# Kernel tuning notes

Hardware: AMD Instinct MI355X
Metric: run time of the kernel (lower is better)

The kernel has to match this reference:

```python
import jax, jax.numpy as jnp
import numpy as np

VOCAB = 32000
DIM = 1024
DEPTH = 4
SEQ = 512
HEADS = 16
NMB = 4
MAXMEM = NMB * SEQ  # 2048
RAMP = 128
COEF = 1e-06
B = 4
DH = DIM // HEADS


def _ln(x, g, b):
    mu = jnp.mean(x, axis=-1, keepdims=True)
    v = jnp.mean((x - mu) ** 2, axis=-1, keepdims=True)
    return (x - mu) / jnp.sqrt(v + 1e-5) * g + b


def setup_inputs() -> dict:
    key = jax.random.key(0)
    ks = jax.random.split(key, 24)
    s = 0.02
    inp = {
        'tokens': jax.random.randint(ks[0], (B, SEQ), 0, VOCAB),
        'mems': jax.random.normal(ks[1], (DEPTH, B, MAXMEM, DIM), jnp.float32) * s,
        'times': jax.random.randint(ks[2], (DEPTH, MAXMEM), 0, 4096, dtype=jnp.int32),
        'token_emb': jax.random.normal(ks[3], (VOCAB, DIM), jnp.float32) * s,
        'expire_W': jax.random.normal(ks[4], (DEPTH, DIM), jnp.float32) * s,
        'expire_b': jnp.full((DEPTH,), -float(MAXMEM), jnp.float32),  # torch init constant
        'ln1_g': jnp.ones((DEPTH, DIM), jnp.float32),
        'ln1_b': jnp.zeros((DEPTH, DIM), jnp.float32),
        'Wq': jax.random.normal(ks[5], (DEPTH, DIM, DIM), jnp.float32) * s,
        'Wkv': jax.random.normal(ks[6], (DEPTH, DIM, 2 * DIM), jnp.float32) * s,
        'Wo': jax.random.normal(ks[7], (DEPTH, DIM, DIM), jnp.float32) * s,
        'bo': jnp.zeros((DEPTH, DIM), jnp.float32),
        'ln2_g': jnp.ones((DEPTH, DIM), jnp.float32),
        'ln2_b': jnp.zeros((DEPTH, DIM), jnp.float32),
        'W1': jax.random.normal(ks[8], (DEPTH, DIM, 4 * DIM), jnp.float32) * s,
        'b1': jnp.zeros((DEPTH, 4 * DIM), jnp.float32),
        'W2': jax.random.normal(ks[9], (DEPTH, 4 * DIM, DIM), jnp.float32) * s,
        'b2': jnp.zeros((DEPTH, DIM), jnp.float32),
        'logits_W': jax.random.normal(ks[10], (DIM, VOCAB), jnp.float32) * s,
        'logits_b': jnp.zeros((VOCAB,), jnp.float32),
    }
    return inp


def reference(tokens, mems, times, token_emb, expire_W, expire_b, ln1_g, ln1_b,
              Wq, Wkv, Wo, bo, ln2_g, ln2_b, W1, b1, W2, b2, logits_W, logits_b):
    n, M = SEQ, MAXMEM
    scale = DH ** -0.5
    x = token_emb[tokens]  # (B, n, DIM)
    # causal mask over concat(mem, x): query i may attend key j iff j <= i + M
    causal = jnp.triu(jnp.ones((n, M + n), bool), k=M + 1)  # True = masked
    aux = jnp.float32(0.0)
    new_mems, new_times = [], []
    tnew = jnp.arange(n - 1, -1, -1, dtype=times.dtype)
    for d in range(DEPTH):
        mem = mems[d]                       # (B, M, DIM)
        t = times[d].astype(jnp.float32)    # (M,)
        hidden = x
        # --- expire span: per-memory-slot soft retention mask ---
        exps = jax.nn.sigmoid(mem @ expire_W[d] + expire_b[d]) * M  # (B, M)
        r = exps[:, None, None, :] - t[None, None, None, :]          # (B,1,1,M)
        r = jnp.pad(r, ((0, 0), (0, 0), (0, 0), (0, n)), constant_values=1.0)
        emask = jnp.clip(r / RAMP + 1.0, 0.0, 1.0)                   # (B,1,1,M+n)
        # --- pre-norm causal attention over concat(mem, x_normed) ---
        xn = _ln(x, ln1_g[d], ln1_b[d])
        q = (xn @ Wq[d]).reshape(B, n, HEADS, DH).transpose(0, 2, 1, 3)
        ctx = jnp.concatenate([mem, xn], axis=1)                     # (B, M+n, DIM)
        kv = ctx @ Wkv[d]
        k = kv[..., :DIM].reshape(B, M + n, HEADS, DH).transpose(0, 2, 1, 3)
        v = kv[..., DIM:].reshape(B, M + n, HEADS, DH).transpose(0, 2, 1, 3)
        dots = jnp.einsum('bhid,bhjd->bhij', q, k) * scale
        dots = jnp.where(causal, -jnp.inf, dots)
        attn = jax.nn.softmax(dots, axis=-1) * emask
        out = jnp.einsum('bhij,bhjd->bhid', attn, v)
        out = out.transpose(0, 2, 1, 3).reshape(B, n, DIM)
        x = out @ Wo[d] + bo[d] + x
        # --- pre-norm FFN ---
        xn2 = _ln(x, ln2_g[d], ln2_b[d])
        x = jax.nn.gelu(xn2 @ W1[d] + b1[d], approximate=False) @ W2[d] + b2[d] + x
        aux = aux + (exps / SEQ).sum() * COEF
        # --- memory bookkeeping (detached) ---
        new_mems.append(jax.lax.stop_gradient(
            jnp.concatenate([mem, hidden], axis=1)[:, -M:]))
        new_times.append(jnp.concatenate([times[d] + n, tnew])[-M:])
    logits = x @ logits_W + logits_b
    return (logits, jnp.stack(new_mems), jnp.stack(new_times), aux)
```

## Files before the change

kernel.cpp:

```cpp
#include <hip/hip_runtime.h>
#include <cmath>

#define DIMC   1024
#define SEQC   512
#define BC     4
#define MC     2048
#define CTXC   2560
#define HEADSC 16
#define DHC    64
#define VOCABC 32000
#define MAXC   512

using short8 = __attribute__((ext_vector_type(8))) short;
using f32x4  = __attribute__((ext_vector_type(4))) float;
using u16x4  = __attribute__((ext_vector_type(4))) unsigned short;
using u16x8  = __attribute__((ext_vector_type(8))) unsigned short;

__device__ __forceinline__ unsigned short f2bf(float f) {
    unsigned u = __float_as_uint(f);
    unsigned r = (u + 0x7fffu + ((u >> 16) & 1u)) >> 16;
    return (unsigned short)r;
}

__device__ __forceinline__ void glds16(const unsigned short* g, char* l) {
    __builtin_amdgcn_global_load_lds(
        (const __attribute__((address_space(1))) void*)g,
        (__attribute__((address_space(3))) void*)l, 16, 0, 0);
}

__global__ __launch_bounds__(256) void embed_kernel(const int* __restrict__ tokens,
                                                    const float* __restrict__ emb,
                                                    float* __restrict__ x) {
    int row = blockIdx.x;
    int tok = tokens[row];
    const float4 v = *(const float4*)(emb + (size_t)tok * DIMC + threadIdx.x * 4);
    *(float4*)(x + (size_t)row * DIMC + threadIdx.x * 4) = v;
}

__global__ __launch_bounds__(256) void times_init_kernel(const int* __restrict__ times,
                                                         float* __restrict__ out_times,
                                                         float* __restrict__ aux) {
    int i = blockIdx.x * 256 + threadIdx.x;
    if (i == 0) aux[0] = 0.0f;
    if (i < 4 * MC) {
        int d = i >> 11, m = i & (MC - 1);
        out_times[i] = (m < MC - SEQC) ? (float)(times[d * MC + SEQC + m] + SEQC)
                                       : (float)(MC - 1 - m);
    }
}

#define PREP_MEM 8192
#define PREP_XC  10240
#define PREP_LN  12288
#define PREP_TOT 24576
__global__ __launch_bounds__(256) void prep_kernel(
    const float* __restrict__ mem_d, const float* __restrict__ x,
    const float* __restrict__ eW, const float* __restrict__ eb,
    float* __restrict__ exps, float* __restrict__ aux,
    unsigned short* __restrict__ mem_b, float* __restrict__ out_mems_d,
    const float* __restrict__ g1, const float* __restrict__ b1v,
    unsigned short* __restrict__ xn_b,
    const float* __restrict__ Wq, const float* __restrict__ Wkv,
    const float* __restrict__ Wo, const float* __restrict__ W1,
    const float* __restrict__ W2,
    unsigned short* __restrict__ wq_t, unsigned short* __restrict__ wkv_t,
    unsigned short* __restrict__ wo_t, unsigned short* __restrict__ w1_t,
    unsigned short* __restrict__ w2_t) {
    __shared__ float sh[1056];
    const int bid = blockIdx.x, tid = threadIdx.x;
    if (bid < PREP_MEM) {
        int row = bid;
        int m = row & 2047, b = row >> 11;
        const float4 v = *(const float4*)(mem_d + (size_t)row * DIMC + tid * 4);
        const float4 w = *(const float4*)(eW + tid * 4);
        float s = v.x * w.x + v.y * w.y + v.z * w.z + v.w * w.w;
        for (int off = 32; off; off >>= 1) s += __shfl_down(s, off, 64);
        int wid = tid >> 6, lane = tid & 63;
        if (lane == 0) sh[wid] = s;
        u16x4 o = { f2bf(v.x), f2bf(v.y), f2bf(v.z), f2bf(v.w) };
        *(u16x4*)(mem_b + (size_t)row * DIMC + tid * 4) = o;
        if (m >= SEQC)
            *(float4*)(out_mems_d + ((size_t)(b * MC + m - SEQC)) * DIMC + tid * 4) = v;
        __syncthreads();
        if (tid == 0) {
            float z = sh[0] + sh[1] + sh[2] + sh[3] + eb[0];
            float e = (float)MC / (1.0f + expf(-z));
            exps[row] = e;
            atomicAdd(aux, e * (1e-6f / (float)SEQC));
        }
    } else if (bid < PREP_XC) {
        int r = bid - PREP_MEM;
        int b = r >> 9, i = r & 511;
        const float4 v = *(const float4*)(x + (size_t)r * DIMC + tid * 4);
        *(float4*)(out_mems_d + ((size_t)(b * MC + MC - SEQC + i)) * DIMC + tid * 4) = v;
    } else if (bid < PREP_LN) {
        int row = bid - PREP_XC;
        const float4 v = *(const float4*)(x + (size_t)row * DIMC + tid * 4);
        float s = v.x + v.y + v.z + v.w;
        float q = v.x * v.x + v.y * v.y + v.z * v.z + v.w * v.w;
        for (int off = 32; off; off >>= 1) {
            s += __shfl_down(s, off, 64);
            q += __shfl_down(q, off, 64);
        }
        int wid = tid >> 6, lane = tid & 63;
        if (lane == 0) { sh[wid] = s; sh[4 + wid] = q; }
        __syncthreads();
        if (tid == 0) {
            float S = sh[0] + sh[1] + sh[2] + sh[3];
            float Q = sh[4] + sh[5] + sh[6] + sh[7];
            float mu = S / DIMC;
            float var = Q / DIMC - mu * mu;
            sh[8] = mu;
            sh[9] = rsqrtf(var + 1e-5f);
        }
        __syncthreads();
        float mu = sh[8], rstd = sh[9];
        const float4 gg = *(const float4*)(g1 + tid * 4);
        const float4 bb = *(const float4*)(b1v + tid * 4);
        u16x4 o = { f2bf((v.x - mu) * rstd * gg.x + bb.x),
                    f2bf((v.y - mu) * rstd * gg.y + bb.y),
                    f2bf((v.z - mu) * rstd * gg.z + bb.z),
                    f2bf((v.w - mu) * rstd * gg.w + bb.w) };
        *(u16x4*)(xn_b + (size_t)row * DIMC + tid * 4) = o;
    } else {
        int t = bid - PREP_LN;
        const float* W; unsigned short* Wt; int K, N, tx, ty;
        if (t < 1024)      { W = Wq;  Wt = wq_t;  K = 1024; N = 1024; tx = t & 31;  ty = t >> 5; }
        else if (t < 3072) { int u = t - 1024; W = Wkv; Wt = wkv_t; K = 1024; N = 2048; tx = u & 63;  ty = u >> 6; }
        else if (t < 4096) { int u = t - 3072; W = Wo;  Wt = wo_t;  K = 1024; N = 1024; tx = u & 31;  ty = u >> 5; }
        else if (t < 8192) { int u = t - 4096; W = W1;  Wt = w1_t;  K = 1024; N = 4096; tx = u & 127; ty = u >> 7; }
        else               { int u = t - 8192; W = W2;  Wt = w2_t;  K = 4096; N = 1024; tx = u & 31;  ty = u >> 5; }
        int n0 = tx * 32, k0 = ty * 32;
        int r = tid >> 3, c = (tid & 7) * 4;
        const float4 v = *(const float4*)(W + (size_t)(k0 + r) * N + n0 + c);
        sh[r * 33 + c] = v.x; sh[r * 33 + c + 1] = v.y;
        sh[r * 33 + c + 2] = v.z; sh[r * 33 + c + 3] = v.w;
        __syncthreads();
        u16x4 o = { f2bf(sh[(c + 0) * 33 + r]), f2bf(sh[(c + 1) * 33 + r]),
                    f2bf(sh[(c + 2) * 33 + r]), f2bf(sh[(c + 3) * 33 + r]) };
        *(u16x4*)(Wt + (size_t)(n0 + r) * K + k0 + c) = o;
    }
}

__global__ __launch_bounds__(64) void compact_kernel(
    const float* __restrict__ exps, const int* __restrict__ times_d,
    int* __restrict__ cidx, float* __restrict__ em_c, int* __restrict__ cnt) {
    int b = blockIdx.x, lane = threadIdx.x;
    int c = 0;
    for (int it = 0; it < 32; ++it) {
        int j = it * 64 + lane;
        float e = exps[b * MC + j];
        float rr = (e - (float)times_d[j]) * (1.0f / 128.0f) + 1.0f;
        float em = fminf(fmaxf(rr, 0.0f), 1.0f);
        unsigned long long mk = __ballot(em > 0.0f);
        int pos = c + __popcll(mk & ((1ull << lane) - 1ull));
        if (em > 0.0f) {
            cidx[b * 2048 + pos] = j;
            em_c[b * 2048 + pos] = em;
        }
        c += __popcll(mk);
    }
    int padded = (c + 63) & ~63;
    int fill_to = padded < MAXC ? MAXC : padded;
    for (int p = c + lane; p < fill_to; p += 64) {
        cidx[b * 2048 + p] = 0;
        em_c[b * 2048 + p] = 0.0f;
    }
    int tiles = padded >> 6;
    if (tiles > (MAXC >> 6)) tiles = MAXC >> 6;
    if (lane == 0) cnt[b] = tiles;
}

__global__ __launch_bounds__(256) void ln_kernel(const float* __restrict__ in,
                                                 const float* __restrict__ g,
                                                 const float* __restrict__ b,
                                                 unsigned short* __restrict__ outb) {
    int row = blockIdx.x;
    int tid = threadIdx.x;
    const float4 v = *(const float4*)(in + (size_t)row * DIMC + tid * 4);
    float s = v.x + v.y + v.z + v.w;
    float q = v.x * v.x + v.y * v.y + v.z * v.z + v.w * v.w;
    for (int off = 32; off; off >>= 1) {
        s += __shfl_down(s, off, 64);
        q += __shfl_down(q, off, 64);
    }
    __shared__ float ss[4], sq[4];
    int wid = tid >> 6, lane = tid & 63;
    if (lane == 0) { ss[wid] = s; sq[wid] = q; }
    __syncthreads();
    if (tid == 0) {
        float S = ss[0] + ss[1] + ss[2] + ss[3];
        float Q = sq[0] + sq[1] + sq[2] + sq[3];
        float mu = S / DIMC;
        float var = Q / DIMC - mu * mu;
        ss[0] = mu;
        sq[0] = rsqrtf(var + 1e-5f);
    }
    __syncthreads();
    float mu = ss[0], rstd = sq[0];
    const float4 gg = *(const float4*)(g + tid * 4);
    const float4 bb = *(const float4*)(b + tid * 4);
    u16x4 o = { f2bf((v.x - mu) * rstd * gg.x + bb.x),
                f2bf((v.y - mu) * rstd * gg.y + bb.y),
                f2bf((v.z - mu) * rstd * gg.z + bb.z),
                f2bf((v.w - mu) * rstd * gg.w + bb.w) };
    *(u16x4*)(outb + (size_t)row * DIMC + tid * 4) = o;
}

__global__ __launch_bounds__(256) void wt_kernel(const float* __restrict__ W,
                                                 unsigned short* __restrict__ Wt,
                                                 int K, int N) {
    __shared__ float t[32][33];
    int tid = threadIdx.x;
    int n0 = blockIdx.x * 32, k0 = blockIdx.y * 32;
    int r = tid >> 3, c = (tid & 7) * 4;
    const float4 v = *(const float4*)(W + (size_t)(k0 + r) * N + n0 + c);
    t[r][c] = v.x; t[r][c + 1] = v.y; t[r][c + 2] = v.z; t[r][c + 3] = v.w;
    __syncthreads();
    u16x4 o = { f2bf(t[c + 0][r]), f2bf(t[c + 1][r]),
                f2bf(t[c + 2][r]), f2bf(t[c + 3][r]) };
    *(u16x4*)(Wt + (size_t)(n0 + r) * K + k0 + c) = o;
}

__global__ __launch_bounds__(256) void vt_kernel(const unsigned short* __restrict__ kvb,
                                                 unsigned short* __restrict__ vT) {
    __shared__ unsigned short t[64][72];
    int jt = blockIdx.x, dt = blockIdx.y, b = blockIdx.z;
    int j0 = MC + jt * 64;
    int tid = threadIdx.x;
    int r = tid >> 3, c = (tid & 7) * 8;
    #pragma unroll
    for (int p = 0; p < 2; ++p) {
        u16x8 v = *(const u16x8*)(kvb + ((size_t)(b * CTXC + j0 + r + p * 32)) * 2048
                                  + 1024 + dt * 64 + c);
        *(u16x8*)&t[r + p * 32][c] = v;
    }
    __syncthreads();
    #pragma unroll
    for (int p = 0; p < 2; ++p) {
        int dr = r + p * 32;
        u16x8 o = { t[c + 0][dr], t[c + 1][dr], t[c + 2][dr], t[c + 3][dr],
                    t[c + 4][dr], t[c + 5][dr], t[c + 6][dr], t[c + 7][dr] };
        *(u16x8*)(vT + ((size_t)(b * 1024 + dt * 64 + dr)) * CTXC + j0 + c) = o;
    }
}

__global__ __launch_bounds__(256) void vtc_kernel(const unsigned short* __restrict__ kvc,
                                                  const int* __restrict__ cnt,
                                                  unsigned short* __restrict__ vTc) {
    int ct = blockIdx.x, dt = blockIdx.y, b = blockIdx.z;
    if (ct >= cnt[b]) return;
    __shared__ unsigned short t[64][72];
    int tid = threadIdx.x;
    int r = tid >> 3, c = (tid & 7) * 8;
    #pragma unroll
    for (int p = 0; p < 2; ++p) {
        u16x8 v = *(const u16x8*)(kvc + ((size_t)(b * MAXC + ct * 64 + r + p * 32)) * 1024
                                  + dt * 64 + c);
        *(u16x8*)&t[r + p * 32][c] = v;
    }
    __syncthreads();
    #pragma unroll
    for (int p = 0; p < 2; ++p) {
        int dr = r + p * 32;
        u16x8 o = { t[c + 0][dr], t[c + 1][dr], t[c + 2][dr], t[c + 3][dr],
                    t[c + 4][dr], t[c + 5][dr], t[c + 6][dr], t[c + 7][dr] };
        *(u16x8*)(vTc + ((size_t)(b * 1024 + dt * 64 + dr)) * MAXC + ct * 64 + c) = o;
    }
}

template<int AMODE, bool BIAS, bool GELU, bool RES, int OMODE, int RT>
__device__ __forceinline__ void gemm_body(
    unsigned short* As, unsigned short* Bs,
    const unsigned short* __restrict__ A, const int* __restrict__ gidx,
    const unsigned short* __restrict__ Wt, const float* __restrict__ bias,
    const float* __restrict__ res, float* __restrict__ Cf,
    unsigned short* __restrict__ Cb, int K, int N, int bx, int by) {
    constexpr int MF = RT / 32;
    const int tid = threadIdx.x;
    const int lane = tid & 63, wave = tid >> 6;
    const int row0 = by * RT, col0 = bx * 128;

    const int seg = tid & 3;
    const int rr0 = tid >> 2;
    const unsigned short* arow[RT / 64];
    #pragma unroll
    for (int p = 0; p < RT / 64; ++p) {
        int r = row0 + p * 64 + rr0;
        if (AMODE == 2) {
            int b = r >> 9, slot = r & (MAXC - 1);
            arow[p] = A + ((size_t)(b * 2048 + gidx[b * 2048 + slot])) * K;
        } else {
            arow[p] = A + (size_t)r * K;
        }
        arow[p] += seg * 8;
    }
    const unsigned short* brow[2];
    #pragma unroll
    for (int p = 0; p < 2; ++p)
        brow[p] = Wt + (size_t)(col0 + p * 64 + rr0) * K + seg * 8;

    char* lA0 = (char*)As + (tid & 192) * 16;
    char* lB0 = (char*)Bs + (tid & 192) * 16;
    char* lB1 = lB0 + 4096;

    f32x4 acc[MF][4] = {};

    const int wr = (wave >> 1) * (RT / 2), wc = (wave & 1) * 64;
    const int fr = lane & 15;
    const int k8 = (lane >> 4) * 8;
    const unsigned short* Ar = As + (size_t)(wr + fr) * 32 + k8;
    const unsigned short* Br = Bs + (size_t)(wc + fr) * 32 + k8;

    for (int k0 = 0; k0 < K; k0 += 32) {
        glds16(arow[0] + k0, lA0);
        if (RT == 128) glds16(arow[1] + k0, lA0 + 4096);
        glds16(brow[0] + k0, lB0);
        glds16(brow[1] + k0, lB1);
        __syncthreads();
        short8 a[MF], b[4];
        #pragma unroll
        for (int m = 0; m < MF; ++m) a[m] = *(const short8*)(Ar + m * 16 * 32);
        #pragma unroll
        for (int n = 0; n < 4; ++n) b[n] = *(const short8*)(Br + n * 16 * 32);
        #pragma unroll
        for (int m = 0; m < MF; ++m)
            #pragma unroll
            for (int n = 0; n < 4; ++n)
                acc[m][n] = __builtin_amdgcn_mfma_f32_16x16x32_bf16(a[m], b[n], acc[m][n], 0, 0, 0);
        __syncthreads();
    }

    const int orow = row0 + wr + (lane >> 4) * 4;
    const int ocol = col0 + wc + fr;
    #pragma unroll
    for (int n = 0; n < 4; ++n) {
        int c = ocol + n * 16;
        float bv = BIAS ? bias[c] : 0.0f;
        #pragma unroll
        for (int m = 0; m < MF; ++m) {
            #pragma unroll
            for (int i = 0; i < 4; ++i) {
                int r0 = orow + m * 16 + i;
                size_t orr = r0;
                if (OMODE == 1) orr = (size_t)r0 + (size_t)(r0 >> 11) * 512;
                if (OMODE == 2) orr = (size_t)r0 + (size_t)(r0 >> 9) * 2048 + 2048;
                size_t idx = orr * N + c;
                float v = acc[m][n][i] + bv;
                if (GELU) v = 0.5f * v * (1.0f + erff(v * 0.70710678118f));
                if (RES) v += res[idx];
                if (Cf) Cf[idx] = v;
                if (Cb) Cb[idx] = f2bf(v);
            }
        }
    }
}

__global__ __launch_bounds__(256) void qkv_gemm_kernel(
    const unsigned short* __restrict__ xn_b, const unsigned short* __restrict__ mem_b,
    const unsigned short* __restrict__ wq_t, const unsigned short* __restrict__ wkv_t,
    const int* __restrict__ cidx, const int* __restrict__ cnt,
    unsigned short* __restrict__ qb, unsigned short* __restrict__ kvb,
    unsigned short* __restrict__ kvc) {
    __shared__ unsigned short As[128 * 32];
    __shared__ unsigned short Bs[128 * 32];
    int id = blockIdx.x;
    if (id < 128) {
        gemm_body<0, false, false, false, 0, 128>(As, Bs, xn_b, nullptr, wq_t,
            nullptr, nullptr, nullptr, qb, 1024, 1024, id & 7, id >> 3);
    } else if (id < 384) {
        id -= 128;
        gemm_body<0, false, false, false, 2, 128>(As, Bs, xn_b, nullptr, wkv_t,
            nullptr, nullptr, nullptr, kvb, 1024, 2048, id & 15, id >> 4);
    } else if (id < 896) {
        id -= 384;
        gemm_body<0, false, false, false, 1, 128>(As, Bs, mem_b, nullptr, wkv_t,
            nullptr, nullptr, nullptr, kvb, 1024, 2048, id & 7, id >> 3);
    } else {
        id -= 896;
        int by = id >> 3;
        int b = (by * 64) >> 9, slot0 = (by * 64) & (MAXC - 1);
        if (slot0 >= cnt[b] * 64) return;
        gemm_body<2, false, false, false, 0, 64>(As, Bs, mem_b, cidx,
            wkv_t + (size_t)1024 * 1024, nullptr, nullptr, nullptr, kvc,
            1024, 1024, id & 7, by);
    }
}

__global__ __launch_bounds__(256) void gemm64_kernel(
    const unsigned short* __restrict__ A, const unsigned short* __restrict__ Wt,
    const float* __restrict__ bias, const float* __restrict__ res,
    float* __restrict__ Cf, unsigned short* __restrict__ Cb, int K) {
    __shared__ unsigned short As[64 * 32];
    __shared__ unsigned short Bs[128 * 32];
    gemm_body<0, true, false, true, 0, 64>(As, Bs, A, nullptr, Wt, bias, res,
        Cf, Cb, K, 1024, blockIdx.x, blockIdx.y);
}

__global__ __launch_bounds__(256) void ffn1_kernel(
    const unsigned short* __restrict__ A, const unsigned short* __restrict__ Wt,
    const float* __restrict__ bias, unsigned short* __restrict__ Cb) {
    __shared__ unsigned short As[128 * 32];
    __shared__ unsigned short Bs[128 * 32];
    gemm_body<0, true, true, false, 0, 128>(As, Bs, A, nullptr, Wt, bias, nullptr,
        nullptr, Cb, 1024, 4096, blockIdx.x, blockIdx.y);
}

__global__ __launch_bounds__(256) void logits_kernel(
    const unsigned short* __restrict__ A, const unsigned short* __restrict__ Wt,
    const float* __restrict__ bias, float* __restrict__ Cf) {
    __shared__ unsigned short As[128 * 32];
    __shared__ unsigned short Bs[128 * 32];
    gemm_body<0, true, false, false, 0, 128>(As, Bs, A, nullptr, Wt, bias, nullptr,
        Cf, nullptr, 1024, VOCABC, blockIdx.y, blockIdx.x);
}

__global__ __launch_bounds__(512) void attn_mfma_kernel(
    const unsigned short* __restrict__ qb,
    const unsigned short* __restrict__ kvb,
    const unsigned short* __restrict__ vT,
    const unsigned short* __restrict__ vTc,
    const int* __restrict__ cidx,
    const float* __restrict__ em_c,
    const int* __restrict__ cnt,
    unsigned short* __restrict__ outb) {
    __shared__ unsigned short K_s[2][64 * 64];
    __shared__ unsigned short V_s[2][64 * 64];
    __shared__ unsigned short p_s[8][16][72];
    __shared__ float em_s[64];
    const int tid = threadIdx.x;
    const int lane = tid & 63, wave = tid >> 6;
    const int qt = blockIdx.x, h = blockIdx.y, b = blockIdx.z;
    const int fr = lane & 15, g = lane >> 4;
    const int gq = qt * 128 + wave * 16;

    short8 aq[2];
    {
        const unsigned short* qp = qb + ((size_t)(b * SEQC + gq + fr)) * DIMC + h * DHC + g * 8;
        aq[0] = *(const short8*)qp;
        aq[1] = *(const short8*)(qp + 32);
    }

    const int sr = tid >> 3, ss = tid & 7;
    const int sw = (ss ^ (sr & 7)) * 8;
    const int wbase = (tid & 448) * 16;

    f32x4 acc_o[4] = {};
    float m_q = -1e30f, l_q = 0.0f;

    const int nlt = 2 * (qt + 1);
    const int nt = 32 + nlt;

    auto stage12 = [&](int t, int q) {
        const int jbase = t * 64;
        glds16(kvb + ((size_t)(b * CTXC + jbase + sr)) * 2048 + h * DHC + sw,
               (char*)K_s[q] + wbase);
        if (t >= 32)
            glds16(vT + ((size_t)(b * 1024 + h * DHC + sr)) * CTXC + jbase + sw,
                   (char*)V_s[q] + wbase);
    };

    stage12(0, 0);
    asm volatile("s_waitcnt vmcnt(0)" ::: "memory");
    __builtin_amdgcn_s_barrier();
    int cur = 0;
    for (int t = 0; t < nt; ++t) {
        if (t + 1 < nt) stage12(t + 1, cur ^ 1);
        if (t + 1 >= nt)      asm volatile("s_waitcnt vmcnt(0)" ::: "memory");
        else if (t >= 31)     asm volatile("s_waitcnt vmcnt(2)" ::: "memory");
        else                  asm volatile("s_waitcnt vmcnt(1)" ::: "memory");
        __builtin_amdgcn_s_barrier();
        __builtin_amdgcn_sched_barrier(0);

        const bool live = (t < 32) || ((t - 32) * 64 <= gq + 15);
        if (live) {
            f32x4 sT[4] = {};
            #pragma unroll
            for (int ks = 0; ks < 2; ++ks)
                #pragma unroll
                for (int mf = 0; mf < 4; ++mf) {
                    int row = mf * 16 + fr, sg = (ks * 4 + g) ^ (row & 7);
                    short8 kk = *(const short8*)((const char*)K_s[cur] + row * 128 + sg * 16);
                    sT[mf] = __builtin_amdgcn_mfma_f32_16x16x32_bf16(kk, aq[ks], sT[mf], 0, 0, 0);
                }

            if (t < 32) {
                float mx = sT[0][0];
                #pragma unroll
                for (int mf = 0; mf < 4; ++mf)
                    #pragma unroll
                    for (int i = 0; i < 4; ++i) mx = fmaxf(mx, sT[mf][i]);
                mx *= 0.125f;
                mx = fmaxf(mx, __shfl_xor(mx, 16, 64));
                mx = fmaxf(mx, __shfl_xor(mx, 32, 64));
                float mnew = fmaxf(m_q, mx);
                float fs = __expf(m_q - mnew);
                m_q = mnew;
                float ps = 0.0f;
                #pragma unroll
                for (int mf = 0; mf < 4; ++mf)
                    #pragma unroll
                    for (int i = 0; i < 4; ++i)
                        ps += __expf(sT[mf][i] * 0.125f - mnew);
                ps += __shfl_xor(ps, 16, 64);
                ps += __shfl_xor(ps, 32, 64);
                l_q = l_q * fs + ps;
            } else {
                const int lt = t - 32;
                const int kq = gq + fr - lt * 64;
                float sv[4][4];
                #pragma unroll
                for (int mf = 0; mf < 4; ++mf)
                    #pragma unroll
                    for (int i = 0; i < 4; ++i) {
                        int kl = mf * 16 + g * 4 + i;
                        sv[mf][i] = (kl <= kq) ? sT[mf][i] * 0.125f : -1e30f;
                    }
                float mx = sv[0][0];
                #pragma unroll
                for (int mf = 0; mf < 4; ++mf)
                    #pragma unroll
                    for (int i = 0; i < 4; ++i) mx = fmaxf(mx, sv[mf][i]);
                mx = fmaxf(mx, __shfl_xor(mx, 16, 64));
                mx = fmaxf(mx, __shfl_xor(mx, 32, 64));
                float mnew = fmaxf(m_q, mx);
                float fs = __expf(m_q - mnew);
                m_q = mnew;
                float ps = 0.0f;
                #pragma unroll
                for (int mf = 0; mf < 4; ++mf)
                    #pragma unroll
                    for (int i = 0; i < 4; ++i) {
                        float pe = __expf(sv[mf][i] - mnew);
                        ps += pe;
                        p_s[wave][fr][mf * 16 + g * 4 + i] = f2bf(pe);
                    }
                ps += __shfl_xor(ps, 16, 64);
                ps += __shfl_xor(ps, 32, 64);
                l_q = l_q * fs + ps;
                float fsr[4];
                #pragma unroll
                for (int i = 0; i < 4; ++i) fsr[i] = __shfl(fs, g * 4 + i, 64);
                #pragma unroll
                for (int n = 0; n < 4; ++n)
                    #pragma unroll
                    for (int i = 0; i < 4; ++i) acc_o[n][i] *= fsr[i];
                asm volatile("s_waitcnt lgkmcnt(0)" ::: "memory");
                #pragma unroll
                for (int ks = 0; ks < 2; ++ks) {
                    short8 ap = *(const short8*)&p_s[wave][fr][ks * 32 + g * 8];
                    #pragma unroll
                    for (int n = 0; n < 4; ++n) {
                        int row = n * 16 + fr, sg = (ks * 4 + g) ^ (row & 7);
                        short8 bv = *(const short8*)((const char*)V_s[cur] + row * 128 + sg * 16);
                        acc_o[n] = __builtin_amdgcn_mfma_f32_16x16x32_bf16(ap, bv, acc_o[n], 0, 0, 0);
                    }
                }
            }
        }
        __builtin_amdgcn_s_barrier();
        cur ^= 1;
    }

    const int nct = cnt[b];
    for (int ct = 0; ct < nct; ++ct) {
        __syncthreads();
        {
            int row = cidx[b * 2048 + ct * 64 + sr];
            glds16(kvb + ((size_t)(b * CTXC + row)) * 2048 + h * DHC + sw,
                   (char*)K_s[0] + wbase);
            glds16(vTc + ((size_t)(b * 1024 + h * DHC + sr)) * MAXC + ct * 64 + sw,
                   (char*)V_s[0] + wbase);
        }
        if (tid < 64) em_s[tid] = em_c[b * 2048 + ct * 64 + tid];
        __syncthreads();
        f32x4 sT[4] = {};
        #pragma unroll
        for (int ks = 0; ks < 2; ++ks)
            #pragma unroll
            for (int mf = 0; mf < 4; ++mf) {
                int row = mf * 16 + fr, sg = (ks * 4 + g) ^ (row & 7);
                short8 kk = *(const short8*)((const char*)K_s[0] + row * 128 + sg * 16);
                sT[mf] = __builtin_amdgcn_mfma_f32_16x16x32_bf16(kk, aq[ks], sT[mf], 0, 0, 0);
            }
        #pragma unroll
        for (int mf = 0; mf < 4; ++mf)
            #pragma unroll
            for (int i = 0; i < 4; ++i) {
                int key = mf * 16 + g * 4 + i;
                float pe = __expf(sT[mf][i] * 0.125f - m_q) * em_s[key];
                p_s[wave][fr][key] = f2bf(pe);
            }
        asm volatile("s_waitcnt lgkmcnt(0)" ::: "memory");
        #pragma unroll
        for (int ks = 0; ks < 2; ++ks) {
            short8 ap = *(const short8*)&p_s[wave][fr][ks * 32 + g * 8];
            #pragma unroll
            for (int n = 0; n < 4; ++n) {
                int row = n * 16 + fr, sg = (ks * 4 + g) ^ (row & 7);
                short8 bv = *(const short8*)((const char*)V_s[0] + row * 128 + sg * 16);
                acc_o[n] = __builtin_amdgcn_mfma_f32_16x16x32_bf16(ap, bv, acc_o[n], 0, 0, 0);
            }
        }
    }

    float linv = 1.0f / l_q;
    float invr[4];
    #pragma unroll
    for (int i = 0; i < 4; ++i) invr[i] = __shfl(linv, g * 4 + i, 64);
    #pragma unroll
    for (int n = 0; n < 4; ++n) {
        #pragma unroll
        for (int i = 0; i < 4; ++i) {
            size_t idx = ((size_t)(b * SEQC + gq + g * 4 + i)) * DIMC + h * DHC + n * 16 + fr;
            outb[idx] = f2bf(acc_o[n][i] * invr[i]);
        }
    }
}

__global__ void aux_write_kernel(const float* __restrict__ aux, float* __restrict__ dst) {
    dst[0] = aux[0];
}

extern "C" void kernel_launch(void* const* d_in, const int* in_sizes, int n_in,
                              void* d_out, int out_size, void* d_ws, size_t ws_size,
                              hipStream_t stream) {
    const int*   tokens    = (const int*)d_in[0];
    const float* mems      = (const float*)d_in[1];
    const int*   times     = (const int*)d_in[2];
    const float* token_emb = (const float*)d_in[3];
    const float* expire_W  = (const float*)d_in[4];
    const float* expire_b  = (const float*)d_in[5];
    const float* ln1_g     = (const float*)d_in[6];
    const float* ln1_b     = (const float*)d_in[7];
    const float* Wq        = (const float*)d_in[8];
    const float* Wkv       = (const float*)d_in[9];
    const float* Wo        = (const float*)d_in[10];
    const float* bo        = (const float*)d_in[11];
    const float* ln2_g     = (const float*)d_in[12];
    const float* ln2_b     = (const float*)d_in[13];
    const float* W1        = (const float*)d_in[14];
    const float* b1        = (const float*)d_in[15];
    const float* W2        = (const float*)d_in[16];
    const float* b2        = (const float*)d_in[17];
    const float* logits_W  = (const float*)d_in[18];
    const float* logits_b  = (const float*)d_in[19];

    float* out = (float*)d_out;
    float* ws  = (float*)d_ws;

    float* x = ws;
    unsigned short* qb_b  = (unsigned short*)(ws + 2097152);
    unsigned short* kv_b  = (unsigned short*)(ws + 3145728);
    unsigned short* vT    = (unsigned short*)(ws + 13631488);
    unsigned short* xn_b  = (unsigned short*)(ws + 18874368);
    unsigned short* attn_b= (unsigned short*)(ws + 19922944);
    unsigned short* ffn_b = (unsigned short*)(ws + 20971520);
    unsigned short* mem_b = (unsigned short*)(ws + 25165824);
    unsigned short* x_b   = (unsigned short*)(ws + 29360128);
    unsigned short* wq_t  = (unsigned short*)(ws + 30408704);
    unsigned short* wkv_t = (unsigned short*)(ws + 30932992);
    unsigned short* wo_t  = (unsigned short*)(ws + 31981568);
    unsigned short* w1_t  = (unsigned short*)(ws + 32505856);
    unsigned short* w2_t  = (unsigned short*)(ws + 34603008);
    float* exps = ws + 36700160;
    float* aux  = ws + 36708352;
    unsigned short* vTc = (unsigned short*)(ws + 36708368);
    unsigned short* kvc = (unsigned short*)(ws + 37756944);
    int*   cidx = (int*)(ws + 38805520);
    float* em_c = ws + 38813712;
    int*   cnt  = (int*)(ws + 38821904);
    unsigned short* lw_t = (unsigned short*)(ws + 2097152);

    float* out_logits = out;
    float* out_mems   = out + 65536000;
    float* out_times  = out + 99090432;

    embed_kernel<<<BC * SEQC, 256, 0, stream>>>(tokens, token_emb, x);
    times_init_kernel<<<32, 256, 0, stream>>>(times, out_times, aux);

    for (int d = 0; d < 4; ++d) {
        const float* mem_d = mems + (size_t)d * BC * MC * DIMC;
        prep_kernel<<<PREP_TOT, 256, 0, stream>>>(
            mem_d, x, expire_W + d * DIMC, expire_b + d, exps, aux,
            mem_b, out_mems + (size_t)d * BC * MC * DIMC,
            ln1_g + d * DIMC, ln1_b + d * DIMC, xn_b,
            Wq + (size_t)d * DIMC * DIMC, Wkv + (size_t)d * DIMC * 2 * DIMC,
            Wo + (size_t)d * DIMC * DIMC, W1 + (size_t)d * DIMC * 4 * DIMC,
            W2 + (size_t)d * 4 * DIMC * DIMC,
            wq_t, wkv_t, wo_t, w1_t, w2_t);
        compact_kernel<<<BC, 64, 0, stream>>>(exps, times + d * MC, cidx, em_c, cnt);
        qkv_gemm_kernel<<<1152, 256, 0, stream>>>(xn_b, mem_b, wq_t, wkv_t,
                                                  cidx, cnt, qb_b, kv_b, kvc);
        vt_kernel<<<dim3(8, 16, BC), 256, 0, stream>>>(kv_b, vT);
        vtc_kernel<<<dim3(MAXC / 64, 16, BC), 256, 0, stream>>>(kvc, cnt, vTc);
        attn_mfma_kernel<<<dim3(4, HEADSC, BC), 512, 0, stream>>>(
            qb_b, kv_b, vT, vTc, cidx, em_c, cnt, attn_b);
        gemm64_kernel<<<dim3(8, 32), 256, 0, stream>>>(
            attn_b, wo_t, bo + d * DIMC, x, x, nullptr, DIMC);
        ln_kernel<<<BC * SEQC, 256, 0, stream>>>(x, ln2_g + d * DIMC, ln2_b + d * DIMC, xn_b);
        ffn1_kernel<<<dim3(32, 16), 256, 0, stream>>>(xn_b, w1_t, b1 + d * 4 * DIMC, ffn_b);
        if (d < 3) {
            gemm64_kernel<<<dim3(8, 32), 256, 0, stream>>>(
                ffn_b, w2_t, b2 + d * DIMC, x, x, nullptr, 4 * DIMC);
        } else {
            gemm64_kernel<<<dim3(8, 32), 256, 0, stream>>>(
                ffn_b, w2_t, b2 + d * DIMC, x, nullptr, x_b, 4 * DIMC);
        }
    }

    wt_kernel<<<dim3(1000, 32), 256, 0, stream>>>(logits_W, lw_t, DIMC, VOCABC);
    logits_kernel<<<dim3(16, 250), 256, 0, stream>>>(x_b, lw_t, logits_b, out_logits);
    aux_write_kernel<<<1, 1, 0, stream>>>(aux, out + 99098624);
}
```

Baseline: 1.760 ms.

## Double-buffer GEMM LDS staging, write V transposed from GEMM epilogue, swizzle logits tiles

The shared GEMM body now double-buffers its LDS tiles. It issues the next k-slice's global-to-LDS loads before computing the current one, using explicit vmcnt waits and raw barriers in place of two __syncthreads per iteration. The QKV GEMM splits K and V computation: mem-row K goes to a narrower kv buffer, while V for the current tokens and the compacted memory rows is written directly in transposed layout from new epilogue modes. This removes the separate vt/vtc transpose kernels and the full mem V projection. The logits kernel remaps block ids to improve L2 reuse. LDS use doubles per block, which may reduce occupancy.

```diff
diff --git a/kernel.cpp b/kernel.cpp
--- a/kernel.cpp
+++ b/kernel.cpp
@@ -222,53 +222,6 @@
     *(u16x4*)(Wt + (size_t)(n0 + r) * K + k0 + c) = o;
 }
 
-__global__ __launch_bounds__(256) void vt_kernel(const unsigned short* __restrict__ kvb,
-                                                 unsigned short* __restrict__ vT) {
-    __shared__ unsigned short t[64][72];
-    int jt = blockIdx.x, dt = blockIdx.y, b = blockIdx.z;
-    int j0 = MC + jt * 64;
-    int tid = threadIdx.x;
-    int r = tid >> 3, c = (tid & 7) * 8;
-    #pragma unroll
-    for (int p = 0; p < 2; ++p) {
-        u16x8 v = *(const u16x8*)(kvb + ((size_t)(b * CTXC + j0 + r + p * 32)) * 2048
-                                  + 1024 + dt * 64 + c);
-        *(u16x8*)&t[r + p * 32][c] = v;
-    }
-    __syncthreads();
-    #pragma unroll
-    for (int p = 0; p < 2; ++p) {
-        int dr = r + p * 32;
-        u16x8 o = { t[c + 0][dr], t[c + 1][dr], t[c + 2][dr], t[c + 3][dr],
-                    t[c + 4][dr], t[c + 5][dr], t[c + 6][dr], t[c + 7][dr] };
-        *(u16x8*)(vT + ((size_t)(b * 1024 + dt * 64 + dr)) * CTXC + j0 + c) = o;
-    }
-}
-
-__global__ __launch_bounds__(256) void vtc_kernel(const unsigned short* __restrict__ kvc,
-                                                  const int* __restrict__ cnt,
-                                                  unsigned short* __restrict__ vTc) {
-    int ct = blockIdx.x, dt = blockIdx.y, b = blockIdx.z;
-    if (ct >= cnt[b]) return;
-    __shared__ unsigned short t[64][72];
-    int tid = threadIdx.x;
-    int r = tid >> 3, c = (tid & 7) * 8;
-    #pragma unroll
-    for (int p = 0; p < 2; ++p) {
-        u16x8 v = *(const u16x8*)(kvc + ((size_t)(b * MAXC + ct * 64 + r + p * 32)) * 1024
-                                  + dt * 64 + c);
-        *(u16x8*)&t[r + p * 32][c] = v;
-    }
-    __syncthreads();
-    #pragma unroll
-    for (int p = 0; p < 2; ++p) {
-        int dr = r + p * 32;
-        u16x8 o = { t[c + 0][dr], t[c + 1][dr], t[c + 2][dr], t[c + 3][dr],
-                    t[c + 4][dr], t[c + 5][dr], t[c + 6][dr], t[c + 7][dr] };
-        *(u16x8*)(vTc + ((size_t)(b * 1024 + dt * 64 + dr)) * MAXC + ct * 64 + c) = o;
-    }
-}
-
 template<int AMODE, bool BIAS, bool GELU, bool RES, int OMODE, int RT>
 __device__ __forceinline__ void gemm_body(
     unsigned short* As, unsigned short* Bs,
@@ -300,24 +253,38 @@
     for (int p = 0; p < 2; ++p)
         brow[p] = Wt + (size_t)(col0 + p * 64 + rr0) * K + seg * 8;
 
-    char* lA0 = (char*)As + (tid & 192) * 16;
-    char* lB0 = (char*)Bs + (tid & 192) * 16;
-    char* lB1 = lB0 + 4096;
+    char* lA = (char*)As + (tid & 192) * 16;
+    char* lB = (char*)Bs + (tid & 192) * 16;
+
+    auto stage = [&](int k0, int q) {
+        char* a = lA + q * (RT * 64);
+        glds16(arow[0] + k0, a);
+        if (RT == 128) glds16(arow[1] + k0, a + 4096);
+        char* bp = lB + q * 8192;
+        glds16(brow[0] + k0, bp);
+        glds16(brow[1] + k0, bp + 4096);
+    };
 
     f32x4 acc[MF][4] = {};
 
     const int wr = (wave >> 1) * (RT / 2), wc = (wave & 1) * 64;
     const int fr = lane & 15;
     const int k8 = (lane >> 4) * 8;
-    const unsigned short* Ar = As + (size_t)(wr + fr) * 32 + k8;
-    const unsigned short* Br = Bs + (size_t)(wc + fr) * 32 + k8;
-
+
+    stage(0, 0);
+    int cur = 0;
     for (int k0 = 0; k0 < K; k0 += 32) {
-        glds16(arow[0] + k0, lA0);
-        if (RT == 128) glds16(arow[1] + k0, lA0 + 4096);
-        glds16(brow[0] + k0, lB0);
-        glds16(brow[1] + k0, lB1);
-        __syncthreads();
+        if (k0 + 32 < K) {
+            stage(k0 + 32, cur ^ 1);
+            if (RT == 128) asm volatile("s_waitcnt vmcnt(4)" ::: "memory");
+            else           asm volatile("s_waitcnt vmcnt(3)" ::: "memory");
+        } else {
+            asm volatile("s_waitcnt vmcnt(0)" ::: "memory");
+        }
+        __builtin_amdgcn_s_barrier();
+        __builtin_amdgcn_sched_barrier(0);
+        const unsigned short* Ar = As + cur * (RT * 32) + (size_t)(wr + fr) * 32 + k8;
+        const unsigned short* Br = Bs + cur * (128 * 32) + (size_t)(wc + fr) * 32 + k8;
         short8 a[MF], b[4];
         #pragma unroll
         for (int m = 0; m < MF; ++m) a[m] = *(const short8*)(Ar + m * 16 * 32);
@@ -328,11 +295,30 @@
             #pragma unroll
             for (int n = 0; n < 4; ++n)
                 acc[m][n] = __builtin_amdgcn_mfma_f32_16x16x32_bf16(a[m], b[n], acc[m][n], 0, 0, 0);
-        __syncthreads();
+        __builtin_amdgcn_s_barrier();
+        cur ^= 1;
     }
 
     const int orow = row0 + wr + (lane >> 4) * 4;
     const int ocol = col0 + wc + fr;
+    if (OMODE >= 3) {
+        #pragma unroll
+        for (int n = 0; n < 4; ++n) {
+            int c = ocol + n * 16;
+            #pragma unroll
+            for (int m = 0; m < MF; ++m) {
+                int r0 = orow + m * 16;
+                int b = r0 >> 9, i = r0 & 511;
+                size_t addr = (OMODE == 3)
+                    ? ((size_t)(b * 1024 + c)) * 512 + i
+                    : ((size_t)(b * 1024 + c)) * MAXC + i;
+                u16x4 o = { f2bf(acc[m][n][0]), f2bf(acc[m][n][1]),
+                            f2bf(acc[m][n][2]), f2bf(acc[m][n][3]) };
+                *(u16x4*)(Cb + addr) = o;
+            }
+        }
+        return;
+    }
     #pragma unroll
     for (int n = 0; n < 4; ++n) {
         int c = ocol + n * 16;
@@ -361,28 +347,33 @@
     const unsigned short* __restrict__ wq_t, const unsigned short* __restrict__ wkv_t,
     const int* __restrict__ cidx, const int* __restrict__ cnt,
     unsigned short* __restrict__ qb, unsigned short* __restrict__ kvb,
-    unsigned short* __restrict__ kvc) {
-    __shared__ unsigned short As[128 * 32];
-    __shared__ unsigned short Bs[128 * 32];
+    unsigned short* __restrict__ vTl, unsigned short* __restrict__ vTc) {
+    __shared__ unsigned short As[2 * 128 * 32];
+    __shared__ unsigned short Bs[2 * 128 * 32];
     int id = blockIdx.x;
     if (id < 128) {
         gemm_body<0, false, false, false, 0, 128>(As, Bs, xn_b, nullptr, wq_t,
             nullptr, nullptr, nullptr, qb, 1024, 1024, id & 7, id >> 3);
-    } else if (id < 384) {
+    } else if (id < 256) {
         id -= 128;
         gemm_body<0, false, false, false, 2, 128>(As, Bs, xn_b, nullptr, wkv_t,
-            nullptr, nullptr, nullptr, kvb, 1024, 2048, id & 15, id >> 4);
+            nullptr, nullptr, nullptr, kvb, 1024, 1024, id & 7, id >> 3);
+    } else if (id < 768) {
+        id -= 256;
+        gemm_body<0, false, false, false, 1, 128>(As, Bs, mem_b, nullptr, wkv_t,
+            nullptr, nullptr, nullptr, kvb, 1024, 1024, id & 7, id >> 3);
     } else if (id < 896) {
-        id -= 384;
-        gemm_body<0, false, false, false, 1, 128>(As, Bs, mem_b, nullptr, wkv_t,
-            nullptr, nullptr, nullptr, kvb, 1024, 2048, id & 7, id >> 3);
+        id -= 768;
+        gemm_body<0, false, false, false, 3, 128>(As, Bs, xn_b, nullptr,
+            wkv_t + (size_t)1024 * 1024, nullptr, nullptr, nullptr, vTl,
+            1024, 1024, id & 7, id >> 3);
     } else {
         id -= 896;
         int by = id >> 3;
         int b = (by * 64) >> 9, slot0 = (by * 64) & (MAXC - 1);
         if (slot0 >= cnt[b] * 64) return;
-        gemm_body<2, false, false, false, 0, 64>(As, Bs, mem_b, cidx,
-            wkv_t + (size_t)1024 * 1024, nullptr, nullptr, nullptr, kvc,
+        gemm_body<2, false, false, false, 4, 64>(As, Bs, mem_b, cidx,
+            wkv_t + (size_t)1024 * 1024, nullptr, nullptr, nullptr, vTc,
             1024, 1024, id & 7, by);
     }
 }
@@ -391,8 +382,8 @@
     const unsigned short* __restrict__ A, const unsigned short* __restrict__ Wt,
     const float* __restrict__ bias, const float* __restrict__ res,
     float* __restrict__ Cf, unsigned short* __restrict__ Cb, int K) {
-    __shared__ unsigned short As[64 * 32];
-    __shared__ unsigned short Bs[128 * 32];
+    __shared__ unsigned short As[2 * 64 * 32];
+    __shared__ unsigned short Bs[2 * 128 * 32];
     gemm_body<0, true, false, true, 0, 64>(As, Bs, A, nullptr, Wt, bias, res,
         Cf, Cb, K, 1024, blockIdx.x, blockIdx.y);
 }
@@ -400,8 +391,8 @@
 __global__ __launch_bounds__(256) void ffn1_kernel(
     const unsigned short* __restrict__ A, const unsigned short* __restrict__ Wt,
     const float* __restrict__ bias, unsigned short* __restrict__ Cb) {
-    __shared__ unsigned short As[128 * 32];
-    __shared__ unsigned short Bs[128 * 32];
+    __shared__ unsigned short As[2 * 128 * 32];
+    __shared__ unsigned short Bs[2 * 128 * 32];
     gemm_body<0, true, true, false, 0, 128>(As, Bs, A, nullptr, Wt, bias, nullptr,
         nullptr, Cb, 1024, 4096, blockIdx.x, blockIdx.y);
 }
@@ -409,16 +400,18 @@
 __global__ __launch_bounds__(256) void logits_kernel(
     const unsigned short* __restrict__ A, const unsigned short* __restrict__ Wt,
     const float* __restrict__ bias, float* __restrict__ Cf) {
-    __shared__ unsigned short As[128 * 32];
-    __shared__ unsigned short Bs[128 * 32];
+    __shared__ unsigned short As[2 * 128 * 32];
+    __shared__ unsigned short Bs[2 * 128 * 32];
+    int D = blockIdx.y * 16 + blockIdx.x;
+    int wid = (D & 7) * 500 + (D >> 3);
     gemm_body<0, true, false, false, 0, 128>(As, Bs, A, nullptr, Wt, bias, nullptr,
-        Cf, nullptr, 1024, VOCABC, blockIdx.y, blockIdx.x);
+        Cf, nullptr, 1024, VOCABC, wid >> 4, wid & 15);
 }
 
 __global__ __launch_bounds__(512) void attn_mfma_kernel(
     const unsigned short* __restrict__ qb,
     const unsigned short* __restrict__ kvb,
-    const unsigned short* __restrict__ vT,
+    const unsigned short* __restrict__ vTl,
     const unsigned short* __restrict__ vTc,
     const int* __restrict__ cidx,
     const float* __restrict__ em_c,
@@ -453,10 +446,10 @@
 
     auto stage12 = [&](int t, int q) {
         const int jbase = t * 64;
-        glds16(kvb + ((size_t)(b * CTXC + jbase + sr)) * 2048 + h * DHC + sw,
+        glds16(kvb + ((size_t)(b * CTXC + jbase + sr)) * 1024 + h * DHC + sw,
                (char*)K_s[q] + wbase);
         if (t >= 32)
-            glds16(vT + ((size_t)(b * 1024 + h * DHC + sr)) * CTXC + jbase + sw,
+            glds16(vTl + ((size_t)(b * 1024 + h * DHC + sr)) * 512 + (jbase - 2048) + sw,
                    (char*)V_s[q] + wbase);
     };
 
@@ -567,7 +560,7 @@
         __syncthreads();
         {
             int row = cidx[b * 2048 + ct * 64 + sr];
-            glds16(kvb + ((size_t)(b * CTXC + row)) * 2048 + h * DHC + sw,
+            glds16(kvb + ((size_t)(b * CTXC + row)) * 1024 + h * DHC + sw,
                    (char*)K_s[0] + wbase);
             glds16(vTc + ((size_t)(b * 1024 + h * DHC + sr)) * MAXC + ct * 64 + sw,
                    (char*)V_s[0] + wbase);
@@ -652,24 +645,23 @@
     float* x = ws;
     unsigned short* qb_b  = (unsigned short*)(ws + 2097152);
     unsigned short* kv_b  = (unsigned short*)(ws + 3145728);
-    unsigned short* vT    = (unsigned short*)(ws + 13631488);
-    unsigned short* xn_b  = (unsigned short*)(ws + 18874368);
-    unsigned short* attn_b= (unsigned short*)(ws + 19922944);
-    unsigned short* ffn_b = (unsigned short*)(ws + 20971520);
-    unsigned short* mem_b = (unsigned short*)(ws + 25165824);
-    unsigned short* x_b   = (unsigned short*)(ws + 29360128);
-    unsigned short* wq_t  = (unsigned short*)(ws + 30408704);
-    unsigned short* wkv_t = (unsigned short*)(ws + 30932992);
-    unsigned short* wo_t  = (unsigned short*)(ws + 31981568);
-    unsigned short* w1_t  = (unsigned short*)(ws + 32505856);
-    unsigned short* w2_t  = (unsigned short*)(ws + 34603008);
-    float* exps = ws + 36700160;
-    float* aux  = ws + 36708352;
-    unsigned short* vTc = (unsigned short*)(ws + 36708368);
-    unsigned short* kvc = (unsigned short*)(ws + 37756944);
-    int*   cidx = (int*)(ws + 38805520);
-    float* em_c = ws + 38813712;
-    int*   cnt  = (int*)(ws + 38821904);
+    unsigned short* vTl   = (unsigned short*)(ws + 8388608);
+    unsigned short* vTc   = (unsigned short*)(ws + 9437184);
+    unsigned short* xn_b  = (unsigned short*)(ws + 10485760);
+    unsigned short* attn_b= (unsigned short*)(ws + 11534336);
+    unsigned short* ffn_b = (unsigned short*)(ws + 12582912);
+    unsigned short* mem_b = (unsigned short*)(ws + 16777216);
+    unsigned short* x_b   = (unsigned short*)(ws + 20971520);
+    unsigned short* wq_t  = (unsigned short*)(ws + 22020096);
+    unsigned short* wkv_t = (unsigned short*)(ws + 22544384);
+    unsigned short* wo_t  = (unsigned short*)(ws + 23592960);
+    unsigned short* w1_t  = (unsigned short*)(ws + 24117248);
+    unsigned short* w2_t  = (unsigned short*)(ws + 26214400);
+    float* exps = ws + 28311552;
+    float* aux  = ws + 28319744;
+    int*   cidx = (int*)(ws + 28319760);
+    float* em_c = ws + 28327952;
+    int*   cnt  = (int*)(ws + 28336144);
     unsigned short* lw_t = (unsigned short*)(ws + 2097152);
 
     float* out_logits = out;
@@ -691,11 +683,9 @@
             wq_t, wkv_t, wo_t, w1_t, w2_t);
         compact_kernel<<<BC, 64, 0, stream>>>(exps, times + d * MC, cidx, em_c, cnt);
         qkv_gemm_kernel<<<1152, 256, 0, stream>>>(xn_b, mem_b, wq_t, wkv_t,
-                                                  cidx, cnt, qb_b, kv_b, kvc);
-        vt_kernel<<<dim3(8, 16, BC), 256, 0, stream>>>(kv_b, vT);
-        vtc_kernel<<<dim3(MAXC / 64, 16, BC), 256, 0, stream>>>(kvc, cnt, vTc);
+                                                  cidx, cnt, qb_b, kv_b, vTl, vTc);
         attn_mfma_kernel<<<dim3(4, HEADSC, BC), 512, 0, stream>>>(
-            qb_b, kv_b, vT, vTc, cidx, em_c, cnt, attn_b);
+            qb_b, kv_b, vTl, vTc, cidx, em_c, cnt, attn_b);
         gemm64_kernel<<<dim3(8, 32), 256, 0, stream>>>(
             attn_b, wo_t, bo + d * DIMC, x, x, nullptr, DIMC);
         ln_kernel<<<BC * SEQC, 256, 0, stream>>>(x, ln2_g + d * DIMC, ln2_b + d * DIMC, xn_b);
```

New measurement: 1.731 ms. Within noise of the previous version (-1.7%).
